# Optimization experiments

Hardware: AMD Instinct MI355X
Metric: run time of the kernel (lower is better)

Reference implementation:

```python
import jax, jax.numpy as jnp
import numpy as np

N_NODES = 100_000
N_EDGES = 1_600_000
NUM_GRAPHS = 512
D1, D2, D3, D5, NUM_CLASSES = 3, 50, 15, 10, 6
BN_EPS = 1e-5


def setup_inputs() -> dict:
    key = jax.random.key(0)
    ks = jax.random.split(key, 16)

    def w(k, shape):
        fan_in = shape[0]
        return jax.random.normal(k, shape, jnp.float32) / np.sqrt(fan_in).astype(np.float32)

    return {
        "x": jax.random.normal(ks[0], (N_NODES, D1), jnp.float32),
        "edge_attr": jax.random.normal(ks[1], (N_EDGES, D1), jnp.float32),
        # edge MLP: Lin(9,50) -> ReLU -> Lin(50,15)
        "edge_w1": w(ks[2], (3 * D1, D2)), "edge_b1": jnp.zeros((D2,), jnp.float32),
        "edge_w2": w(ks[3], (D2, D3)), "edge_b2": jnp.zeros((D3,), jnp.float32),
        # node MLP: Lin(18,50) -> ReLU -> Lin(50,15)
        "node_w1": w(ks[4], (D1 + D3, D2)), "node_b1": jnp.zeros((D2,), jnp.float32),
        "node_w2": w(ks[5], (D2, D3)), "node_b2": jnp.zeros((D3,), jnp.float32),
        # readout head
        "fc1_w": w(ks[6], (D3, D5)), "fc1_b": jnp.zeros((D5,), jnp.float32),
        "bn_gamma": jnp.ones((D5,), jnp.float32), "bn_beta": jnp.zeros((D5,), jnp.float32),
        "fc2_w": w(ks[7], (D5, NUM_CLASSES)), "fc2_b": jnp.zeros((NUM_CLASSES,), jnp.float32),
        # graph structure
        "edge_index": jax.random.randint(ks[8], (2, N_EDGES), 0, N_NODES, jnp.int32),
        "batch": jnp.sort(jax.random.randint(ks[9], (N_NODES,), 0, NUM_GRAPHS, jnp.int32)),
    }


def _segment_mean(vals, idx, num_segments):
    s = jax.ops.segment_sum(vals, idx, num_segments=num_segments)
    c = jax.ops.segment_sum(jnp.ones((vals.shape[0], 1), vals.dtype), idx,
                            num_segments=num_segments)
    return s / jnp.maximum(c, 1.0)


def reference(x, edge_attr,
              edge_w1, edge_b1, edge_w2, edge_b2,
              node_w1, node_b1, node_w2, node_b2,
              fc1_w, fc1_b, bn_gamma, bn_beta, fc2_w, fc2_b,
              edge_index, batch):
    row, col = edge_index[0], edge_index[1]
    # edge model: cat([x[row], x[col], edge_attr]) -> MLP  -> [E, D3]
    e_in = jnp.concatenate([x[row], x[col], edge_attr], axis=1)
    edge_attr2 = jax.nn.relu(e_in @ edge_w1 + edge_b1) @ edge_w2 + edge_b2
    # node model: cat([x[col], edge_attr2]) -> MLP -> scatter_mean over row
    n_in = jnp.concatenate([x[col], edge_attr2], axis=1)  # [E, D1+D3]
    msg = jax.nn.relu(n_in @ node_w1 + node_b1) @ node_w2 + node_b2  # [E, D3]
    x2 = _segment_mean(msg, row, x.shape[0])  # [N, D3]
    # global mean pool per graph -> [G, D3]
    u = _segment_mean(x2, batch, NUM_GRAPHS)
    # head: fc1 -> BatchNorm1d (batch stats) -> relu -> fc2 -> log_softmax
    h = u @ fc1_w + fc1_b
    mu = h.mean(axis=0)
    var = h.var(axis=0)  # biased, matches BN training normalization
    h = bn_gamma * (h - mu) * jax.lax.rsqrt(var + BN_EPS) + bn_beta
    h = jax.nn.relu(h)
    logits = h @ fc2_w + fc2_b
    return jax.nn.log_softmax(logits, axis=1)
```

## Files before the change

### kernel.cpp

```cpp
#include <hip/hip_runtime.h>
#include <hip/hip_bf16.h>
#include <math.h>

#define N_NODES    100000
#define N_EDGES    1600000
#define NUM_GRAPHS 512
#define D2 50
#define D3 15
#define D5 10
#define NCLS 6
#define BN_EPS 1e-5f

#define NBLK1 ((N_NODES + 1023) / 1024)

#define W_EW1T 0
#define W_EW2T 2560
#define W_NW1T 3712
#define W_NW2T 6272
#define W_TOTAL 7680

#define EDGE_BLOCKS 2500
#define EDGE_WAVES  (EDGE_BLOCKS * 4)
#define TILES32     (N_EDGES / 32)
#define EDGE_ITERS  (TILES32 / EDGE_WAVES)

typedef __attribute__((ext_vector_type(8))) short short8;
typedef __attribute__((ext_vector_type(4))) float float4_;
union BU { unsigned u[4]; short8 s; };

__device__ __forceinline__ unsigned short f2bf(float f) {
    __hip_bfloat16 h = __float2bfloat16(f);
    union { __hip_bfloat16 h; unsigned short u; } c; c.h = h; return c.u;
}
__device__ __forceinline__ float bf2f(unsigned short u) {
    union { __hip_bfloat16 h; unsigned short u; } c; c.u = u;
    return __bfloat162float(c.h);
}
__device__ __forceinline__ unsigned int pkbf(float a, float b) {
    return (unsigned int)f2bf(a) | ((unsigned int)f2bf(b) << 16);
}
__device__ __forceinline__ unsigned bp(int s4, unsigned v) {
    return (unsigned)__builtin_amdgcn_ds_bpermute(s4, (int)v);
}

__global__ __launch_bounds__(256) void prep_kernel(
    const float* __restrict__ ew1, const float* __restrict__ eb1,
    const float* __restrict__ ew2, const float* __restrict__ eb2,
    const float* __restrict__ nw1, const float* __restrict__ nb1,
    const float* __restrict__ nw2, const float* __restrict__ nb2,
    unsigned short* __restrict__ wh, unsigned short* __restrict__ wl,
    const float* __restrict__ x, ushort4* __restrict__ x4b,
    const int* __restrict__ edge_index, int* __restrict__ counts)
{
    int gtid = blockIdx.x * 256 + threadIdx.x;
    int gsz = gridDim.x * 256;

    for (int i = gtid; i < W_TOTAL; i += gsz) {
        float v = 0.0f;
        if (i < W_EW2T) {
            int m = i / 40, k = i % 40;
            if (m < 50) {
                if (k < 3)                 v = ew1[k * 50 + m];
                else if (k == 3)           v = eb1[m];
                else if (k >= 4 && k < 7)  v = ew1[(k - 1) * 50 + m];
                else if (k >= 8 && k < 11) v = ew1[(k - 2) * 50 + m];
            }
        } else if (i < W_NW1T) {
            int j = i - W_EW2T; int m = j / 72, k = j % 72;
            if (m < 15) { if (k < 50) v = ew2[k * 15 + m]; else if (k == 50) v = eb2[m]; }
        } else if (i < W_NW2T) {
            int j = i - W_NW1T; int m = j / 40, k = j % 40;
            if (m < 50) {
                if (k < 15)                  v = nw1[(3 + k) * 50 + m];
                else if (k >= 16 && k < 19)  v = nw1[(k - 16) * 50 + m];
                else if (k == 19)            v = nb1[m];
            }
        } else if (i < 7424) {
            int j = i - W_NW2T; int m = j / 72, k = j % 72;
            if (m < 15) { if (k < 50) v = nw2[k * 15 + m]; else if (k == 50) v = nb2[m]; }
        }
        unsigned short h = f2bf(v);
        unsigned short l = f2bf(v - bf2f(h));
        wh[i] = h; wl[i] = l;
    }

    for (int n = gtid; n < N_NODES; n += gsz) {
        ushort4 v;
        v.x = f2bf(x[n * 3 + 0]); v.y = f2bf(x[n * 3 + 1]);
        v.z = f2bf(x[n * 3 + 2]); v.w = 0;
        x4b[n] = v;
    }

    for (int e = gtid; e < N_EDGES; e += gsz)
        atomicAdd(&counts[edge_index[e]], 1);
}

__global__ __launch_bounds__(1024) void scan1_kernel(
    const int* __restrict__ counts, int* __restrict__ scanned, int* __restrict__ bsums)
{
    __shared__ int tmp[1024];
    int i = blockIdx.x * 1024 + threadIdx.x;
    int v = (i < N_NODES) ? counts[i] : 0;
    tmp[threadIdx.x] = v;
    __syncthreads();
    #pragma unroll
    for (int off = 1; off < 1024; off <<= 1) {
        int t = (threadIdx.x >= off) ? tmp[threadIdx.x - off] : 0;
        __syncthreads();
        tmp[threadIdx.x] += t;
        __syncthreads();
    }
    int incl = tmp[threadIdx.x];
    if (i < N_NODES) scanned[i] = incl - v;
    if (threadIdx.x == 1023) bsums[blockIdx.x] = incl;
}

__global__ __launch_bounds__(128) void scan2_kernel(
    const int* __restrict__ bsums, int* __restrict__ bofs)
{
    __shared__ int tmp[128];
    int v = (threadIdx.x < NBLK1) ? bsums[threadIdx.x] : 0;
    tmp[threadIdx.x] = v;
    __syncthreads();
    #pragma unroll
    for (int off = 1; off < 128; off <<= 1) {
        int t = (threadIdx.x >= off) ? tmp[threadIdx.x - off] : 0;
        __syncthreads();
        tmp[threadIdx.x] += t;
        __syncthreads();
    }
    if (threadIdx.x < NBLK1) bofs[threadIdx.x] = tmp[threadIdx.x] - v;
}

__global__ __launch_bounds__(256) void scan3_kernel(
    const int* __restrict__ scanned, const int* __restrict__ bofs,
    int* __restrict__ cursor)
{
    int n = blockIdx.x * 256 + threadIdx.x;
    if (n >= N_NODES) return;
    cursor[n] = scanned[n] + bofs[n >> 10];
}

struct EIn { unsigned w0, w1, w2, w3, h0, h1; int pos; };

__device__ __forceinline__ EIn load_in(int ebase, int n, int quad,
    const int* __restrict__ edge_index, const ushort4* __restrict__ x4b,
    const float* __restrict__ edge_attr, int* __restrict__ cursor)
{
    EIn r; r.w0 = r.w1 = r.w2 = r.w3 = 0; r.h0 = r.h1 = 0; r.pos = 0;
    int e = ebase + n;
    if (quad == 0) {
        int row = edge_index[e];
        int col = edge_index[N_EDGES + e];
        ushort4 xr = x4b[row];
        ushort4 xc = x4b[col];
        r.w0 = (unsigned)xr.x | ((unsigned)xr.y << 16);
        r.w1 = (unsigned)xr.z | (0x3F80u << 16);
        r.w2 = (unsigned)xc.x | ((unsigned)xc.y << 16);
        r.w3 = (unsigned)xc.z;
        r.pos = atomicAdd(&cursor[row], 1);
    } else if (quad == 1) {
        r.w0 = pkbf(edge_attr[e * 3 + 0], edge_attr[e * 3 + 1]);
        r.w1 = (unsigned)f2bf(edge_attr[e * 3 + 2]);
    } else if (quad == 2) {
        int col = edge_index[N_EDGES + e];
        ushort4 xc = x4b[col];
        r.h0 = (unsigned)xc.x | ((unsigned)xc.y << 16);
        r.h1 = (unsigned)xc.z | (0x3F80u << 16);
    }
    return r;
}

__device__ __forceinline__ void perm64(const unsigned U[4][2], int s0, int s1, bool hi,
                                       short8& Bc0, short8& Bc1)
{
    BU b0, b1;
    {
        unsigned a0 = bp(s0, U[0][0]), a1 = bp(s0, U[1][0]);
        unsigned a2 = bp(s0, U[0][1]), a3 = bp(s0, U[1][1]);
        unsigned a4 = bp(s1, U[0][0]), a5 = bp(s1, U[1][0]);
        unsigned a6 = bp(s1, U[0][1]), a7 = bp(s1, U[1][1]);
        b0.u[0] = hi ? a1 : a0;
        b0.u[1] = hi ? a3 : a2;
        b0.u[2] = hi ? a5 : a4;
        b0.u[3] = hi ? a7 : a6;
    }
    {
        unsigned a0 = bp(s0, U[2][0]), a1 = bp(s0, U[3][0]);
        unsigned a2 = bp(s0, U[2][1]), a3 = bp(s0, U[3][1]);
        unsigned a4 = bp(s1, U[2][0]), a5 = bp(s1, U[3][0]);
        unsigned a6 = bp(s1, U[2][1]), a7 = bp(s1, U[3][1]);
        b1.u[0] = hi ? a1 : a0;
        b1.u[1] = hi ? a3 : a2;
        b1.u[2] = hi ? a5 : a4;
        b1.u[3] = hi ? a7 : a6;
    }
    Bc0 = b0.s; Bc1 = b1.s;
}

__device__ __forceinline__ short8 perm16(const unsigned U2[2], int s0, int s1,
                                         int quad, unsigned h0, unsigned h1)
{
    BU d;
    d.u[0] = bp(s0, U2[0]);
    d.u[1] = bp(s0, U2[1]);
    d.u[2] = bp(s1, U2[0]);
    d.u[3] = bp(s1, U2[1]);
    if (quad == 2) { d.u[0] = h0; d.u[1] = h1; d.u[2] = 0; d.u[3] = 0; }
    else if (quad == 3) { d.u[0] = 0; d.u[1] = 0; d.u[2] = 0; d.u[3] = 0; }
    return d.s;
}

__global__ __launch_bounds__(256) void edge_mfma_kernel(
    const unsigned short* __restrict__ wh_g, const unsigned short* __restrict__ wl_g,
    const ushort4* __restrict__ x4b, const float* __restrict__ edge_attr,
    const int* __restrict__ edge_index,
    int* __restrict__ cursor, float* __restrict__ msg)
{
    int tid = threadIdx.x, wave = tid >> 6, lane = tid & 63;
    int n = lane & 15, quad = lane >> 4;

    short8 A1h[4], A1l[4], A3h[4], A3l[4];
    #pragma unroll
    for (int t4 = 0; t4 < 4; t4++) {
        int o1 = W_EW1T + (t4 * 16 + n) * 40 + quad * 8;
        A1h[t4] = *(const short8*)(wh_g + o1);
        A1l[t4] = *(const short8*)(wl_g + o1);
        int o3 = W_NW1T + (t4 * 16 + n) * 40 + quad * 8;
        A3h[t4] = *(const short8*)(wh_g + o3);
        A3l[t4] = *(const short8*)(wl_g + o3);
    }
    short8 A2h[2], A2l[2], A4h[2], A4l[2];
    #pragma unroll
    for (int kc = 0; kc < 2; kc++) {
        int o2 = W_EW2T + n * 72 + kc * 32 + quad * 8;
        A2h[kc] = *(const short8*)(wh_g + o2);
        A2l[kc] = *(const short8*)(wl_g + o2);
        int o4 = W_NW2T + n * 72 + kc * 32 + quad * 8;
        A4h[kc] = *(const short8*)(wh_g + o4);
        A4l[kc] = *(const short8*)(wl_g + o4);
    }

    int s0 = ((quad & 1) * 32 + n) * 4;
    int s1 = s0 + 64;
    bool hi = (quad & 2) != 0;

    int t = blockIdx.x * 4 + wave;
    EIn cur0 = load_in(t * 32,      n, quad, edge_index, x4b, edge_attr, cursor);
    EIn cur1 = load_in(t * 32 + 16, n, quad, edge_index, x4b, edge_attr, cursor);

    for (int it = 0; it < EDGE_ITERS; it++) {
        int p0 = __shfl(cur0.pos, n);
        int p1 = __shfl(cur1.pos, n);

        int tn = t + EDGE_WAVES;
        EIn nx0, nx1;
        nx0.w0 = nx0.w1 = nx0.w2 = nx0.w3 = nx0.h0 = nx0.h1 = 0; nx0.pos = 0;
        nx1 = nx0;
        if (it + 1 < EDGE_ITERS) {
            nx0 = load_in(tn * 32,      n, quad, edge_index, x4b, edge_attr, cursor);
            nx1 = load_in(tn * 32 + 16, n, quad, edge_index, x4b, edge_attr, cursor);
        }

        BU t0, t1;
        t0.u[0] = cur0.w0; t0.u[1] = cur0.w1; t0.u[2] = cur0.w2; t0.u[3] = cur0.w3;
        t1.u[0] = cur1.w0; t1.u[1] = cur1.w1; t1.u[2] = cur1.w2; t1.u[3] = cur1.w3;
        short8 B1a = t0.s, B1b = t1.s;

        unsigned U1a[4][2], U1b[4][2];
        #pragma unroll
        for (int t4 = 0; t4 < 4; t4++) {
            float4_ za = {0.f, 0.f, 0.f, 0.f}, zb = {0.f, 0.f, 0.f, 0.f};
            za = __builtin_amdgcn_mfma_f32_16x16x32_bf16(A1l[t4], B1a, za, 0, 0, 0);
            zb = __builtin_amdgcn_mfma_f32_16x16x32_bf16(A1l[t4], B1b, zb, 0, 0, 0);
            za = __builtin_amdgcn_mfma_f32_16x16x32_bf16(A1h[t4], B1a, za, 0, 0, 0);
            zb = __builtin_amdgcn_mfma_f32_16x16x32_bf16(A1h[t4], B1b, zb, 0, 0, 0);
            U1a[t4][0] = pkbf(fmaxf(za[0], 0.f), fmaxf(za[1], 0.f));
            U1a[t4][1] = pkbf(fmaxf(za[2], 0.f), fmaxf(za[3], 0.f));
            U1b[t4][0] = pkbf(fmaxf(zb[0], 0.f), fmaxf(zb[1], 0.f));
            U1b[t4][1] = pkbf(fmaxf(zb[2], 0.f), fmaxf(zb[3], 0.f));
        }

        short8 B2a0, B2a1, B2b0, B2b1;
        perm64(U1a, s0, s1, hi, B2a0, B2a1);
        perm64(U1b, s0, s1, hi, B2b0, B2b1);
        if (quad == 2) {
            BU fa, fb; fa.s = B2a1; fb.s = B2b1;
            fa.u[1] = (fa.u[1] & 0xFFFF0000u) | 0x3F80u;
            fb.u[1] = (fb.u[1] & 0xFFFF0000u) | 0x3F80u;
            B2a1 = fa.s; B2b1 = fb.s;
        }

        float4_ a2a = {0.f, 0.f, 0.f, 0.f}, a2b = {0.f, 0.f, 0.f, 0.f};
        a2a = __builtin_amdgcn_mfma_f32_16x16x32_bf16(A2l[0], B2a0, a2a, 0, 0, 0);
        a2b = __builtin_amdgcn_mfma_f32_16x16x32_bf16(A2l[0], B2b0, a2b, 0, 0, 0);
        a2a = __builtin_amdgcn_mfma_f32_16x16x32_bf16(A2h[0], B2a0, a2a, 0, 0, 0);
        a2b = __builtin_amdgcn_mfma_f32_16x16x32_bf16(A2h[0], B2b0, a2b, 0, 0, 0);
        a2a = __builtin_amdgcn_mfma_f32_16x16x32_bf16(A2l[1], B2a1, a2a, 0, 0, 0);
        a2b = __builtin_amdgcn_mfma_f32_16x16x32_bf16(A2l[1], B2b1, a2b, 0, 0, 0);
        a2a = __builtin_amdgcn_mfma_f32_16x16x32_bf16(A2h[1], B2a1, a2a, 0, 0, 0);
        a2b = __builtin_amdgcn_mfma_f32_16x16x32_bf16(A2h[1], B2b1, a2b, 0, 0, 0);

        unsigned U2a[2] = { pkbf(a2a[0], a2a[1]), pkbf(a2a[2], a2a[3]) };
        unsigned U2b[2] = { pkbf(a2b[0], a2b[1]), pkbf(a2b[2], a2b[3]) };

        short8 B3a = perm16(U2a, s0, s1, quad, cur0.h0, cur0.h1);
        short8 B3b = perm16(U2b, s0, s1, quad, cur1.h0, cur1.h1);

        unsigned U3a[4][2], U3b[4][2];
        #pragma unroll
        for (int t4 = 0; t4 < 4; t4++) {
            float4_ za = {0.f, 0.f, 0.f, 0.f}, zb = {0.f, 0.f, 0.f, 0.f};
            za = __builtin_amdgcn_mfma_f32_16x16x32_bf16(A3l[t4], B3a, za, 0, 0, 0);
            zb = __builtin_amdgcn_mfma_f32_16x16x32_bf16(A3l[t4], B3b, zb, 0, 0, 0);
            za = __builtin_amdgcn_mfma_f32_16x16x32_bf16(A3h[t4], B3a, za, 0, 0, 0);
            zb = __builtin_amdgcn_mfma_f32_16x16x32_bf16(A3h[t4], B3b, zb, 0, 0, 0);
            U3a[t4][0] = pkbf(fmaxf(za[0], 0.f), fmaxf(za[1], 0.f));
            U3a[t4][1] = pkbf(fmaxf(za[2], 0.f), fmaxf(za[3], 0.f));
            U3b[t4][0] = pkbf(fmaxf(zb[0], 0.f), fmaxf(zb[1], 0.f));
            U3b[t4][1] = pkbf(fmaxf(zb[2], 0.f), fmaxf(zb[3], 0.f));
        }

        short8 B4a0, B4a1, B4b0, B4b1;
        perm64(U3a, s0, s1, hi, B4a0, B4a1);
        perm64(U3b, s0, s1, hi, B4b0, B4b1);
        if (quad == 2) {
            BU fa, fb; fa.s = B4a1; fb.s = B4b1;
            fa.u[1] = (fa.u[1] & 0xFFFF0000u) | 0x3F80u;
            fb.u[1] = (fb.u[1] & 0xFFFF0000u) | 0x3F80u;
            B4a1 = fa.s; B4b1 = fb.s;
        }

        float4_ ma = {0.f, 0.f, 0.f, 0.f}, mb = {0.f, 0.f, 0.f, 0.f};
        ma = __builtin_amdgcn_mfma_f32_16x16x32_bf16(A4l[0], B4a0, ma, 0, 0, 0);
        mb = __builtin_amdgcn_mfma_f32_16x16x32_bf16(A4l[0], B4b0, mb, 0, 0, 0);
        ma = __builtin_amdgcn_mfma_f32_16x16x32_bf16(A4h[0], B4a0, ma, 0, 0, 0);
        mb = __builtin_amdgcn_mfma_f32_16x16x32_bf16(A4h[0], B4b0, mb, 0, 0, 0);
        ma = __builtin_amdgcn_mfma_f32_16x16x32_bf16(A4l[1], B4a1, ma, 0, 0, 0);
        mb = __builtin_amdgcn_mfma_f32_16x16x32_bf16(A4l[1], B4b1, mb, 0, 0, 0);
        ma = __builtin_amdgcn_mfma_f32_16x16x32_bf16(A4h[1], B4a1, ma, 0, 0, 0);
        mb = __builtin_amdgcn_mfma_f32_16x16x32_bf16(A4h[1], B4b1, mb, 0, 0, 0);

        *(float4_*)(msg + (size_t)p0 * 16 + quad * 4) = ma;
        *(float4_*)(msg + (size_t)p1 * 16 + quad * 4) = mb;

        cur0 = nx0; cur1 = nx1; t = tn;
    }
}

__global__ __launch_bounds__(256) void gather_pool_kernel(
    const float* __restrict__ msg, const int* __restrict__ scanned,
    const int* __restrict__ bofs, const int* __restrict__ counts,
    const int* __restrict__ batch, float* __restrict__ gsum)
{
    __shared__ float acc[64 * 16];
    int n0 = blockIdx.x * 256;
    int n = n0 + threadIdx.x;

    float v[16];
    #pragma unroll
    for (int k = 0; k < 16; k++) v[k] = 0.0f;
    if (n < N_NODES) {
        int start = scanned[n] + bofs[n >> 10];
        int deg = counts[n];
        for (int j = 0; j < deg; j++) {
            const float4* mp = (const float4*)(msg + (size_t)(start + j) * 16);
            float4 b0 = mp[0], b1 = mp[1], b2 = mp[2], b3 = mp[3];
            v[0] += b0.x;  v[1] += b0.y;  v[2] += b0.z;  v[3] += b0.w;
            v[4] += b1.x;  v[5] += b1.y;  v[6] += b1.z;  v[7] += b1.w;
            v[8] += b2.x;  v[9] += b2.y;  v[10] += b2.z; v[11] += b2.w;
            v[12] += b3.x; v[13] += b3.y; v[14] += b3.z;
        }
        float inv = 1.0f / fmaxf((float)deg, 1.0f);
        #pragma unroll
        for (int k = 0; k < 15; k++) v[k] *= inv;
        v[15] = 1.0f;
    }

    int gmin = batch[n0];
    int gmax = batch[min(n0 + 255, N_NODES - 1)];
    int range = gmax - gmin + 1;
    if (range <= 64) {
        for (int t = threadIdx.x; t < range * 16; t += 256) acc[t] = 0.0f;
        __syncthreads();
        if (n < N_NODES) {
            int g = batch[n] - gmin;
            float* dst = &acc[g * 16];
            #pragma unroll
            for (int k = 0; k < 16; k++) atomicAdd(&dst[k], v[k]);
        }
        __syncthreads();
        for (int t = threadIdx.x; t < range * 16; t += 256) {
            float w = acc[t];
            if (w != 0.0f) atomicAdd(&gsum[(size_t)gmin * 16 + t], w);
        }
    } else {
        if (n < N_NODES) {
            int g = batch[n];
            float* dst = gsum + (size_t)g * 16;
            #pragma unroll
            for (int k = 0; k < 16; k++) atomicAdd(&dst[k], v[k]);
        }
    }
}

__global__ __launch_bounds__(512) void head_kernel(
    const float* __restrict__ gsum,
    const float* __restrict__ fc1w, const float* __restrict__ fc1b,
    const float* __restrict__ gamma, const float* __restrict__ beta,
    const float* __restrict__ fc2w, const float* __restrict__ fc2b,
    float* __restrict__ out)
{
    __shared__ float ssum[D5], ssq[D5], smu[D5], sistd[D5];
    int g = threadIdx.x;
    if (g < D5) { ssum[g] = 0.0f; ssq[g] = 0.0f; }
    __syncthreads();

    const float* src = gsum + (size_t)g * 16;
    float inv = 1.0f / fmaxf(src[15], 1.0f);
    float u[D3];
    #pragma unroll
    for (int k = 0; k < D3; k++) u[k] = src[k] * inv;

    float h[D5];
    #pragma unroll
    for (int c = 0; c < D5; c++) h[c] = fc1b[c];
    #pragma unroll
    for (int k = 0; k < D3; k++) {
        float v = u[k];
        #pragma unroll
        for (int c = 0; c < D5; c++) h[c] = fmaf(v, fc1w[k * D5 + c], h[c]);
    }

    int lane = threadIdx.x & 63;
    #pragma unroll
    for (int c = 0; c < D5; c++) {
        float v = h[c];
        float v2 = v * v;
        #pragma unroll
        for (int off = 32; off >= 1; off >>= 1) {
            v  += __shfl_xor(v,  off);
            v2 += __shfl_xor(v2, off);
        }
        if (lane == 0) { atomicAdd(&ssum[c], v); atomicAdd(&ssq[c], v2); }
    }
    __syncthreads();
    if (g < D5) {
        float mu = ssum[g] * (1.0f / NUM_GRAPHS);
        float var = ssq[g] * (1.0f / NUM_GRAPHS) - mu * mu;
        smu[g] = mu;
        sistd[g] = rsqrtf(var + BN_EPS);
    }
    __syncthreads();

    float hn[D5];
    #pragma unroll
    for (int c = 0; c < D5; c++) {
        float v = gamma[c] * (h[c] - smu[c]) * sistd[c] + beta[c];
        hn[c] = fmaxf(v, 0.0f);
    }

    float lg[NCLS];
    #pragma unroll
    for (int j = 0; j < NCLS; j++) lg[j] = fc2b[j];
    #pragma unroll
    for (int c = 0; c < D5; c++) {
        float v = hn[c];
        #pragma unroll
        for (int j = 0; j < NCLS; j++) lg[j] = fmaf(v, fc2w[c * NCLS + j], lg[j]);
    }

    float m = lg[0];
    #pragma unroll
    for (int j = 1; j < NCLS; j++) m = fmaxf(m, lg[j]);
    float se = 0.0f;
    #pragma unroll
    for (int j = 0; j < NCLS; j++) se += expf(lg[j] - m);
    float lse = logf(se);
    #pragma unroll
    for (int j = 0; j < NCLS; j++) out[g * NCLS + j] = lg[j] - m - lse;
}

extern "C" void kernel_launch(void* const* d_in, const int* in_sizes, int n_in,
                              void* d_out, int out_size, void* d_ws, size_t ws_size,
                              hipStream_t stream) {
    const float* x         = (const float*)d_in[0];
    const float* edge_attr = (const float*)d_in[1];
    const float* ew1  = (const float*)d_in[2];
    const float* eb1  = (const float*)d_in[3];
    const float* ew2  = (const float*)d_in[4];
    const float* eb2  = (const float*)d_in[5];
    const float* nw1  = (const float*)d_in[6];
    const float* nb1  = (const float*)d_in[7];
    const float* nw2  = (const float*)d_in[8];
    const float* nb2  = (const float*)d_in[9];
    const float* fc1w = (const float*)d_in[10];
    const float* fc1b = (const float*)d_in[11];
    const float* gamma= (const float*)d_in[12];
    const float* beta = (const float*)d_in[13];
    const float* fc2w = (const float*)d_in[14];
    const float* fc2b = (const float*)d_in[15];
    const int* edge_index = (const int*)d_in[16];
    const int* batch      = (const int*)d_in[17];

    char* p = (char*)d_ws;
    float* msg = (float*)p;            p += (size_t)N_EDGES * 16 * sizeof(float);
    int* counts  = (int*)p;            p += (size_t)N_NODES * sizeof(int);
    int* scanned = (int*)p;            p += (size_t)N_NODES * sizeof(int);
    int* cursor  = (int*)p;            p += (size_t)N_NODES * sizeof(int);
    int* bsums   = (int*)p;            p += 128 * sizeof(int);
    int* bofs    = (int*)p;            p += 128 * sizeof(int);
    ushort4* x4b = (ushort4*)p;        p += (size_t)N_NODES * sizeof(ushort4);
    float* gsum  = (float*)p;          p += (size_t)NUM_GRAPHS * 16 * sizeof(float);
    unsigned short* wh = (unsigned short*)p; p += W_TOTAL * sizeof(unsigned short);
    unsigned short* wl = (unsigned short*)p; p += W_TOTAL * sizeof(unsigned short);

    hipMemsetAsync(counts, 0, (size_t)N_NODES * sizeof(int), stream);
    hipMemsetAsync(gsum, 0, (size_t)NUM_GRAPHS * 16 * sizeof(float), stream);

    int egrid = (N_EDGES + 255) / 256;
    int ngrid = (N_NODES + 255) / 256;

    prep_kernel<<<egrid, 256, 0, stream>>>(
        ew1, eb1, ew2, eb2, nw1, nb1, nw2, nb2, wh, wl,
        x, x4b, edge_index, counts);
    scan1_kernel<<<NBLK1, 1024, 0, stream>>>(counts, scanned, bsums);
    scan2_kernel<<<1, 128, 0, stream>>>(bsums, bofs);
    scan3_kernel<<<ngrid, 256, 0, stream>>>(scanned, bofs, cursor);
    edge_mfma_kernel<<<EDGE_BLOCKS, 256, 0, stream>>>(
        wh, wl, x4b, edge_attr, edge_index, cursor, msg);
    gather_pool_kernel<<<ngrid, 256, 0, stream>>>(
        msg, scanned, bofs, counts, batch, gsum);
    head_kernel<<<1, 512, 0, stream>>>(
        gsum, fc1w, fc1b, gamma, beta, fc2w, fc2b, (float*)d_out);
}
```

Measured before the change: 354.5 us.

## Store edge messages as bf16, split MFMA accumulators, and use a wave-shuffle scan

The per-edge message buffer is now written as bf16 instead of fp32, halving the scattered write traffic in the edge kernel and the read traffic in the gather kernel, with bf16 values unpacked by bit shifts when gathered. The hi/lo MFMA chains now accumulate into separate registers and are summed at the end, which shortens the dependent MFMA chain. The block scan is rewritten with wavefront shuffles instead of a shared-memory Hillis-Steele loop with many barriers. The cost is reduced precision of the stored messages before the mean aggregation.

```diff
diff --git a/kernel.cpp b/kernel.cpp
--- a/kernel.cpp
+++ b/kernel.cpp
@@ -27,6 +27,7 @@
 typedef __attribute__((ext_vector_type(8))) short short8;
 typedef __attribute__((ext_vector_type(4))) float float4_;
 union BU { unsigned u[4]; short8 s; };
+union FU { unsigned u; float f; };
 
 __device__ __forceinline__ unsigned short f2bf(float f) {
     __hip_bfloat16 h = __float2bfloat16(f);
@@ -42,6 +43,8 @@
 __device__ __forceinline__ unsigned bp(int s4, unsigned v) {
     return (unsigned)__builtin_amdgcn_ds_bpermute(s4, (int)v);
 }
+__device__ __forceinline__ float lo16(unsigned u) { FU c; c.u = u << 16; return c.f; }
+__device__ __forceinline__ float hi16(unsigned u) { FU c; c.u = u & 0xFFFF0000u; return c.f; }
 
 __global__ __launch_bounds__(256) void prep_kernel(
     const float* __restrict__ ew1, const float* __restrict__ eb1,
@@ -98,19 +101,29 @@
 __global__ __launch_bounds__(1024) void scan1_kernel(
     const int* __restrict__ counts, int* __restrict__ scanned, int* __restrict__ bsums)
 {
-    __shared__ int tmp[1024];
+    __shared__ int wsum[16], wofs[16];
     int i = blockIdx.x * 1024 + threadIdx.x;
+    int lane = threadIdx.x & 63, wid = threadIdx.x >> 6;
     int v = (i < N_NODES) ? counts[i] : 0;
-    tmp[threadIdx.x] = v;
+    int sc = v;
+    #pragma unroll
+    for (int off = 1; off < 64; off <<= 1) {
+        int t = __shfl_up(sc, off);
+        if (lane >= off) sc += t;
+    }
+    if (lane == 63) wsum[wid] = sc;
     __syncthreads();
-    #pragma unroll
-    for (int off = 1; off < 1024; off <<= 1) {
-        int t = (threadIdx.x >= off) ? tmp[threadIdx.x - off] : 0;
-        __syncthreads();
-        tmp[threadIdx.x] += t;
-        __syncthreads();
-    }
-    int incl = tmp[threadIdx.x];
+    if (wid == 0) {
+        int s = (lane < 16) ? wsum[lane] : 0;
+        #pragma unroll
+        for (int off = 1; off < 16; off <<= 1) {
+            int t = __shfl_up(s, off);
+            if (lane >= off) s += t;
+        }
+        if (lane < 16) wofs[lane] = s - wsum[lane];
+    }
+    __syncthreads();
+    int incl = sc + wofs[wid];
     if (i < N_NODES) scanned[i] = incl - v;
     if (threadIdx.x == 1023) bsums[blockIdx.x] = incl;
 }
@@ -215,7 +228,7 @@
     const unsigned short* __restrict__ wh_g, const unsigned short* __restrict__ wl_g,
     const ushort4* __restrict__ x4b, const float* __restrict__ edge_attr,
     const int* __restrict__ edge_index,
-    int* __restrict__ cursor, float* __restrict__ msg)
+    int* __restrict__ cursor, unsigned short* __restrict__ msgb)
 {
     int tid = threadIdx.x, wave = tid >> 6, lane = tid & 63;
     int n = lane & 15, quad = lane >> 4;
@@ -291,18 +304,21 @@
             B2a1 = fa.s; B2b1 = fb.s;
         }
 
-        float4_ a2a = {0.f, 0.f, 0.f, 0.f}, a2b = {0.f, 0.f, 0.f, 0.f};
-        a2a = __builtin_amdgcn_mfma_f32_16x16x32_bf16(A2l[0], B2a0, a2a, 0, 0, 0);
-        a2b = __builtin_amdgcn_mfma_f32_16x16x32_bf16(A2l[0], B2b0, a2b, 0, 0, 0);
-        a2a = __builtin_amdgcn_mfma_f32_16x16x32_bf16(A2h[0], B2a0, a2a, 0, 0, 0);
-        a2b = __builtin_amdgcn_mfma_f32_16x16x32_bf16(A2h[0], B2b0, a2b, 0, 0, 0);
-        a2a = __builtin_amdgcn_mfma_f32_16x16x32_bf16(A2l[1], B2a1, a2a, 0, 0, 0);
-        a2b = __builtin_amdgcn_mfma_f32_16x16x32_bf16(A2l[1], B2b1, a2b, 0, 0, 0);
-        a2a = __builtin_amdgcn_mfma_f32_16x16x32_bf16(A2h[1], B2a1, a2a, 0, 0, 0);
-        a2b = __builtin_amdgcn_mfma_f32_16x16x32_bf16(A2h[1], B2b1, a2b, 0, 0, 0);
-
-        unsigned U2a[2] = { pkbf(a2a[0], a2a[1]), pkbf(a2a[2], a2a[3]) };
-        unsigned U2b[2] = { pkbf(a2b[0], a2b[1]), pkbf(a2b[2], a2b[3]) };
+        float4_ a2al = {0.f, 0.f, 0.f, 0.f}, a2ah = {0.f, 0.f, 0.f, 0.f};
+        float4_ a2bl = {0.f, 0.f, 0.f, 0.f}, a2bh = {0.f, 0.f, 0.f, 0.f};
+        a2al = __builtin_amdgcn_mfma_f32_16x16x32_bf16(A2l[0], B2a0, a2al, 0, 0, 0);
+        a2bl = __builtin_amdgcn_mfma_f32_16x16x32_bf16(A2l[0], B2b0, a2bl, 0, 0, 0);
+        a2ah = __builtin_amdgcn_mfma_f32_16x16x32_bf16(A2h[0], B2a0, a2ah, 0, 0, 0);
+        a2bh = __builtin_amdgcn_mfma_f32_16x16x32_bf16(A2h[0], B2b0, a2bh, 0, 0, 0);
+        a2al = __builtin_amdgcn_mfma_f32_16x16x32_bf16(A2l[1], B2a1, a2al, 0, 0, 0);
+        a2bl = __builtin_amdgcn_mfma_f32_16x16x32_bf16(A2l[1], B2b1, a2bl, 0, 0, 0);
+        a2ah = __builtin_amdgcn_mfma_f32_16x16x32_bf16(A2h[1], B2a1, a2ah, 0, 0, 0);
+        a2bh = __builtin_amdgcn_mfma_f32_16x16x32_bf16(A2h[1], B2b1, a2bh, 0, 0, 0);
+
+        unsigned U2a[2] = { pkbf(a2al[0] + a2ah[0], a2al[1] + a2ah[1]),
+                            pkbf(a2al[2] + a2ah[2], a2al[3] + a2ah[3]) };
+        unsigned U2b[2] = { pkbf(a2bl[0] + a2bh[0], a2bl[1] + a2bh[1]),
+                            pkbf(a2bl[2] + a2bh[2], a2bl[3] + a2bh[3]) };
 
         short8 B3a = perm16(U2a, s0, s1, quad, cur0.h0, cur0.h1);
         short8 B3b = perm16(U2b, s0, s1, quad, cur1.h0, cur1.h1);
@@ -331,25 +347,31 @@
             B4a1 = fa.s; B4b1 = fb.s;
         }
 
-        float4_ ma = {0.f, 0.f, 0.f, 0.f}, mb = {0.f, 0.f, 0.f, 0.f};
-        ma = __builtin_amdgcn_mfma_f32_16x16x32_bf16(A4l[0], B4a0, ma, 0, 0, 0);
-        mb = __builtin_amdgcn_mfma_f32_16x16x32_bf16(A4l[0], B4b0, mb, 0, 0, 0);
-        ma = __builtin_amdgcn_mfma_f32_16x16x32_bf16(A4h[0], B4a0, ma, 0, 0, 0);
-        mb = __builtin_amdgcn_mfma_f32_16x16x32_bf16(A4h[0], B4b0, mb, 0, 0, 0);
-        ma = __builtin_amdgcn_mfma_f32_16x16x32_bf16(A4l[1], B4a1, ma, 0, 0, 0);
-        mb = __builtin_amdgcn_mfma_f32_16x16x32_bf16(A4l[1], B4b1, mb, 0, 0, 0);
-        ma = __builtin_amdgcn_mfma_f32_16x16x32_bf16(A4h[1], B4a1, ma, 0, 0, 0);
-        mb = __builtin_amdgcn_mfma_f32_16x16x32_bf16(A4h[1], B4b1, mb, 0, 0, 0);
-
-        *(float4_*)(msg + (size_t)p0 * 16 + quad * 4) = ma;
-        *(float4_*)(msg + (size_t)p1 * 16 + quad * 4) = mb;
+        float4_ mal = {0.f, 0.f, 0.f, 0.f}, mah = {0.f, 0.f, 0.f, 0.f};
+        float4_ mbl = {0.f, 0.f, 0.f, 0.f}, mbh = {0.f, 0.f, 0.f, 0.f};
+        mal = __builtin_amdgcn_mfma_f32_16x16x32_bf16(A4l[0], B4a0, mal, 0, 0, 0);
+        mbl = __builtin_amdgcn_mfma_f32_16x16x32_bf16(A4l[0], B4b0, mbl, 0, 0, 0);
+        mah = __builtin_amdgcn_mfma_f32_16x16x32_bf16(A4h[0], B4a0, mah, 0, 0, 0);
+        mbh = __builtin_amdgcn_mfma_f32_16x16x32_bf16(A4h[0], B4b0, mbh, 0, 0, 0);
+        mal = __builtin_amdgcn_mfma_f32_16x16x32_bf16(A4l[1], B4a1, mal, 0, 0, 0);
+        mbl = __builtin_amdgcn_mfma_f32_16x16x32_bf16(A4l[1], B4b1, mbl, 0, 0, 0);
+        mah = __builtin_amdgcn_mfma_f32_16x16x32_bf16(A4h[1], B4a1, mah, 0, 0, 0);
+        mbh = __builtin_amdgcn_mfma_f32_16x16x32_bf16(A4h[1], B4b1, mbh, 0, 0, 0);
+
+        uint2 pa, pb;
+        pa.x = pkbf(mal[0] + mah[0], mal[1] + mah[1]);
+        pa.y = pkbf(mal[2] + mah[2], mal[3] + mah[3]);
+        pb.x = pkbf(mbl[0] + mbh[0], mbl[1] + mbh[1]);
+        pb.y = pkbf(mbl[2] + mbh[2], mbl[3] + mbh[3]);
+        *(uint2*)(msgb + (size_t)p0 * 16 + quad * 4) = pa;
+        *(uint2*)(msgb + (size_t)p1 * 16 + quad * 4) = pb;
 
         cur0 = nx0; cur1 = nx1; t = tn;
     }
 }
 
 __global__ __launch_bounds__(256) void gather_pool_kernel(
-    const float* __restrict__ msg, const int* __restrict__ scanned,
+    const unsigned short* __restrict__ msgb, const int* __restrict__ scanned,
     const int* __restrict__ bofs, const int* __restrict__ counts,
     const int* __restrict__ batch, float* __restrict__ gsum)
 {
@@ -364,12 +386,16 @@
         int start = scanned[n] + bofs[n >> 10];
         int deg = counts[n];
         for (int j = 0; j < deg; j++) {
-            const float4* mp = (const float4*)(msg + (size_t)(start + j) * 16);
-            float4 b0 = mp[0], b1 = mp[1], b2 = mp[2], b3 = mp[3];
-            v[0] += b0.x;  v[1] += b0.y;  v[2] += b0.z;  v[3] += b0.w;
-            v[4] += b1.x;  v[5] += b1.y;  v[6] += b1.z;  v[7] += b1.w;
-            v[8] += b2.x;  v[9] += b2.y;  v[10] += b2.z; v[11] += b2.w;
-            v[12] += b3.x; v[13] += b3.y; v[14] += b3.z;
+            const uint4* mp = (const uint4*)(msgb + (size_t)(start + j) * 16);
+            uint4 qa = mp[0], qb = mp[1];
+            v[0]  += lo16(qa.x); v[1]  += hi16(qa.x);
+            v[2]  += lo16(qa.y); v[3]  += hi16(qa.y);
+            v[4]  += lo16(qa.z); v[5]  += hi16(qa.z);
+            v[6]  += lo16(qa.w); v[7]  += hi16(qa.w);
+            v[8]  += lo16(qb.x); v[9]  += hi16(qb.x);
+            v[10] += lo16(qb.y); v[11] += hi16(qb.y);
+            v[12] += lo16(qb.z); v[13] += hi16(qb.z);
+            v[14] += lo16(qb.w);
         }
         float inv = 1.0f / fmaxf((float)deg, 1.0f);
         #pragma unroll
@@ -504,7 +530,7 @@
     const int* batch      = (const int*)d_in[17];
 
     char* p = (char*)d_ws;
-    float* msg = (float*)p;            p += (size_t)N_EDGES * 16 * sizeof(float);
+    unsigned short* msgb = (unsigned short*)p; p += (size_t)N_EDGES * 16 * sizeof(unsigned short);
     int* counts  = (int*)p;            p += (size_t)N_NODES * sizeof(int);
     int* scanned = (int*)p;            p += (size_t)N_NODES * sizeof(int);
     int* cursor  = (int*)p;            p += (size_t)N_NODES * sizeof(int);
@@ -528,9 +554,9 @@
     scan2_kernel<<<1, 128, 0, stream>>>(bsums, bofs);
     scan3_kernel<<<ngrid, 256, 0, stream>>>(scanned, bofs, cursor);
     edge_mfma_kernel<<<EDGE_BLOCKS, 256, 0, stream>>>(
-        wh, wl, x4b, edge_attr, edge_index, cursor, msg);
+        wh, wl, x4b, edge_attr, edge_index, cursor, msgb);
     gather_pool_kernel<<<ngrid, 256, 0, stream>>>(
-        msg, scanned, bofs, counts, batch, gsum);
+        msgb, scanned, bofs, counts, batch, gsum);
     head_kernel<<<1, 512, 0, stream>>>(
         gsum, fc1w, fc1b, gamma, beta, fc2w, fc2b, (float*)d_out);
 }
```

Measured after the change: 373.2 us. 1.05x slower.
